# Optimization experiments

Hardware: AMD Instinct MI355X
Metric: run time of the kernel (lower is better)

## Reference

```python
import jax, jax.numpy as jnp
import numpy as np

# module hyper-parameters (init_kwargs)
DELTA_VAR = 0.75
DELTA_DIST = 2.0
ALPHA, BETA, GAMMA = 1.0, 1.0, 0.001

B, E, H, W, C = 4, 16, 512, 512, 24


def _safe_norm(x, axis):
    # L2 norm with zero (not nan) gradient at 0, matching torch.norm's subgradient
    sq = jnp.sum(x * x, axis=axis)
    safe = jnp.where(sq == 0, 1.0, sq)
    return jnp.where(sq == 0, 0.0, jnp.sqrt(safe))


def setup_inputs() -> dict:
    key = jax.random.key(0)
    k1, k2 = jax.random.split(key)
    input_ = jax.random.normal(k1, (B, E, H, W), dtype=jnp.float32)
    target = jax.random.randint(k2, (B, 1, H, W), 0, C)  # consecutive labels 0..C-1 (w.h.p. all present)
    return {"input_": input_, "target": target, "n_instances": C}


def reference(input_, target, n_instances):
    # Discriminative loss (De Brabandere et al. 2017), math identical to the torch
    # one-hot-expansion version but expressed as segment reductions + gathers.
    Cn = int(n_instances)
    b, e = input_.shape[0], input_.shape[1]
    emb = input_.reshape(b, e, -1).transpose(0, 2, 1)  # (B, N, E)
    tgt = target.reshape(b, -1)                        # (B, N) int labels

    # per-instance cluster means: segment-sum over pixels (the torch code does the
    # same reduction via a dense BxCxExHxW one-hot expansion)
    def _means(e_bn, t_n):
        sums = jax.ops.segment_sum(e_bn, t_n, num_segments=Cn)                      # (C, E)
        counts = jax.ops.segment_sum(jnp.ones(t_n.shape, e_bn.dtype), t_n, num_segments=Cn)  # (C,)
        return sums / counts[:, None], counts

    mu, counts = jax.vmap(_means)(emb, tgt)            # (B, C, E), (B, C)

    # variance term: hinged distance of each pixel embedding to its own cluster mean
    mu_per_pix = jnp.take_along_axis(mu, tgt[:, :, None], axis=1)  # (B, N, E)
    dist = _safe_norm(emb - mu_per_pix, axis=-1)                   # (B, N)
    hinge = jnp.square(jnp.maximum(dist - DELTA_VAR, 0.0))
    var_per_inst = jax.vmap(lambda h, t: jax.ops.segment_sum(h, t, num_segments=Cn))(hinge, tgt) / counts  # (B, C)
    variance_term = jnp.mean(jnp.sum(var_per_inst, axis=1) / Cn)

    # distance term: hinged pairwise repulsion between cluster means
    dmat = _safe_norm(mu[:, :, None, :] - mu[:, None, :, :], axis=-1)  # (B, C, C)
    repulsion = 2.0 * DELTA_DIST * (1.0 - jnp.eye(Cn, dtype=mu.dtype))
    hinged = jnp.square(jnp.maximum(repulsion - dmat, 0.0))
    distance_term = jnp.mean(jnp.sum(hinged, axis=(1, 2))) / (Cn * (Cn - 1))

    # regularizer: mean norm of cluster means
    reg_term = jnp.mean(jnp.sum(_safe_norm(mu, axis=-1), axis=1)) / Cn

    return ALPHA * variance_term + BETA * distance_term + GAMMA * reg_term
```

## Files before the change

### kernel.cpp

```cpp
#include <hip/hip_runtime.h>
#include <cstdint>

#define B_SZ   4
#define E_DIM  16
#define C_INST 24
#define HW_N   262144
#define NG     (HW_N / 4)

#define DELTA_VAR  0.75f
#define DELTA_DIST 2.0f
#define ALPHA_W 1.0f
#define BETA_W  1.0f
#define GAMMA_W 0.001f

#define P1_NB   16
#define P1_ITER (NG / (P1_NB * 256))
#define BUK_STRIDE 25

__global__ __launch_bounds__(256) void pass1_kernel(
    const float* __restrict__ input, const int* __restrict__ target,
    float* __restrict__ sums, float* __restrict__ counts)
{
    __shared__ float buk[256][BUK_STRIDE];
    const int tid = threadIdx.x;
    const int eg  = blockIdx.y;
    const int b   = blockIdx.z;

    float* __restrict__ myrow = &buk[tid][0];
    #pragma unroll
    for (int j = 0; j < C_INST; ++j) myrow[j] = 0.f;

    const int4* __restrict__ tgt4 = (const int4*)(target + (size_t)b * HW_N);
    const int gbase = blockIdx.x * 256 * P1_ITER + tid;

    if (eg < E_DIM) {
        const float4* __restrict__ src4 =
            (const float4*)(input + ((size_t)b * E_DIM + eg) * HW_N);
        int4   lab = tgt4[gbase];
        float4 x   = src4[gbase];
        #pragma unroll
        for (int it = 0; it < P1_ITER; ++it) {
            const int4   labc = lab;
            const float4 xc   = x;
            if (it + 1 < P1_ITER) {
                lab = tgt4[gbase + (it + 1) * 256];
                x   = src4[gbase + (it + 1) * 256];
            }
            myrow[labc.x] += xc.x;
            myrow[labc.y] += xc.y;
            myrow[labc.z] += xc.z;
            myrow[labc.w] += xc.w;
        }
    } else {
        #pragma unroll
        for (int it = 0; it < P1_ITER; ++it) {
            const int4 labc = tgt4[gbase + it * 256];
            myrow[labc.x] += 1.f;
            myrow[labc.y] += 1.f;
            myrow[labc.z] += 1.f;
            myrow[labc.w] += 1.f;
        }
    }
    __syncthreads();

    if (tid < 8 * C_INST) {
        const int c  = tid >> 3;
        const int r0 = tid & 7;
        float s = 0.f;
        #pragma unroll
        for (int i = 0; i < 32; ++i) s += buk[8 * i + r0][c];
        s += __shfl_xor(s, 1, 64);
        s += __shfl_xor(s, 2, 64);
        s += __shfl_xor(s, 4, 64);
        if (r0 == 0) {
            if (eg < E_DIM)
                unsafeAtomicAdd(&sums[((size_t)b * E_DIM + eg) * C_INST + c], s);
            else
                unsafeAtomicAdd(&counts[b * C_INST + c], s);
        }
    }
}

__global__ __launch_bounds__(256) void pass2_kernel(
    const float* __restrict__ input, const int* __restrict__ target,
    const float* __restrict__ sums, const float* __restrict__ counts,
    float* __restrict__ loss_acc)
{
    __shared__ float mu_l[C_INST][20];
    __shared__ float w_l[C_INST];
    __shared__ float redw[4];
    const int tid  = threadIdx.x;
    const int lane = tid & 63;
    const int wv   = tid >> 6;
    const int b    = blockIdx.y;

    if (tid < C_INST) {
        const float cv = counts[b * C_INST + tid];
        w_l[tid] = (cv > 0.f) ? 1.f / cv : 0.f;
    }
    __syncthreads();
    for (int i = tid; i < E_DIM * C_INST; i += 256) {
        const int e = i / C_INST, c = i % C_INST;
        mu_l[c][e] = sums[((size_t)b * E_DIM + e) * C_INST + c] * w_l[c];
    }
    __syncthreads();

    const int g = blockIdx.x * 256 + tid;
    const int4 lab4 = ((const int4*)(target + (size_t)b * HW_N))[g];
    const int lp[4] = {lab4.x, lab4.y, lab4.z, lab4.w};

    const float4* __restrict__ src4 = (const float4*)(input + (size_t)b * E_DIM * HW_N);
    float xs[E_DIM * 4];
    #pragma unroll
    for (int e = 0; e < E_DIM; ++e)
        ((float4*)xs)[e] = src4[(size_t)e * NG + g];

    float vloc = 0.f;
    #pragma unroll
    for (int p = 0; p < 4; ++p) {
        const int c = lp[p];
        float d2 = 0.f;
        #pragma unroll
        for (int e = 0; e < E_DIM; ++e) {
            const float diff = xs[e * 4 + p] - mu_l[c][e];
            d2 = fmaf(diff, diff, d2);
        }
        const float h = fmaxf(sqrtf(d2) - DELTA_VAR, 0.f);
        vloc = fmaf(h * h, w_l[c], vloc);
    }

    #pragma unroll
    for (int m = 1; m < 64; m <<= 1) vloc += __shfl_xor(vloc, m, 64);
    if (lane == 0) redw[wv] = vloc;
    __syncthreads();
    if (tid == 0)
        unsafeAtomicAdd(loss_acc, redw[0] + redw[1] + redw[2] + redw[3]);
}

__global__ __launch_bounds__(256) void final_kernel(
    const float* __restrict__ sums, const float* __restrict__ counts,
    const float* __restrict__ loss_acc, float* __restrict__ out)
{
    __shared__ float mu[B_SZ][C_INST][E_DIM];
    __shared__ float red[256];
    const int tid = threadIdx.x;

    for (int i = tid; i < B_SZ * C_INST * E_DIM; i += 256) {
        const int b = i / (C_INST * E_DIM);
        const int r = i % (C_INST * E_DIM);
        const int e = r / C_INST, c = r % C_INST;
        const float cv = counts[b * C_INST + c];
        mu[b][c][e] = (cv > 0.f)
            ? sums[((size_t)b * E_DIM + e) * C_INST + c] / cv : 0.f;
    }
    __syncthreads();

    float acc = 0.f;
    for (int i = tid; i < B_SZ * C_INST; i += 256) {
        const int b = i / C_INST, c = i % C_INST;
        float n2 = 0.f;
        #pragma unroll
        for (int e = 0; e < E_DIM; ++e) n2 += mu[b][c][e] * mu[b][c][e];
        acc += GAMMA_W * sqrtf(n2) * (1.0f / (B_SZ * C_INST));
    }
    for (int i = tid; i < B_SZ * C_INST * C_INST; i += 256) {
        const int b  = i / (C_INST * C_INST);
        const int r  = i % (C_INST * C_INST);
        const int c1 = r / C_INST, c2 = r % C_INST;
        if (c1 != c2) {
            float d2 = 0.f;
            #pragma unroll
            for (int e = 0; e < E_DIM; ++e) {
                const float d = mu[b][c1][e] - mu[b][c2][e];
                d2 += d * d;
            }
            const float h = fmaxf(2.0f * DELTA_DIST - sqrtf(d2), 0.f);
            acc += BETA_W * h * h * (1.0f / (B_SZ * C_INST * (C_INST - 1)));
        }
    }

    red[tid] = acc;
    __syncthreads();
    for (int s = 128; s > 0; s >>= 1) {
        if (tid < s) red[tid] += red[tid + s];
        __syncthreads();
    }
    if (tid == 0)
        out[0] = red[0] + ALPHA_W * loss_acc[0] * (1.0f / (B_SZ * C_INST));
}

extern "C" void kernel_launch(void* const* d_in, const int* in_sizes, int n_in,
                              void* d_out, int out_size, void* d_ws, size_t ws_size,
                              hipStream_t stream)
{
    const float* input  = (const float*)d_in[0];
    const int*   target = (const int*)d_in[1];

    float* sums     = (float*)d_ws;
    float* counts   = sums + B_SZ * E_DIM * C_INST;
    float* loss_acc = counts + B_SZ * C_INST;
    const size_t ws_bytes =
        (size_t)(B_SZ * E_DIM * C_INST + B_SZ * C_INST + 1) * sizeof(float);
    hipMemsetAsync(d_ws, 0, ws_bytes, stream);

    pass1_kernel<<<dim3(P1_NB, E_DIM + 1, B_SZ), 256, 0, stream>>>(input, target, sums, counts);
    pass2_kernel<<<dim3(NG / 256, B_SZ), 256, 0, stream>>>(input, target, sums, counts, loss_acc);
    final_kernel<<<1, 256, 0, stream>>>(sums, counts, loss_acc, (float*)d_out);
}
```

Before: 131.9 us.

## Process two embedding channels per pass1 block and fold counts into ballot popcounts

Each pass1 block now accumulates two embedding channels, so every label load is reused for twice the data and the number of label reads drops. The dedicated count blocks are removed. Instead, each block counts the labels for a slice of iterations using wave ballot and popcount, and the slice is chosen so that the eight channel-pair blocks together cover every chunk exactly once. This costs a larger shared-memory bucket per thread (stride 51), which may lower occupancy, plus ballot overhead in the iterations that do counting.

```diff
diff --git a/kernel.cpp b/kernel.cpp
--- a/kernel.cpp
+++ b/kernel.cpp
@@ -15,69 +15,90 @@
 
 #define P1_NB   16
 #define P1_ITER (NG / (P1_NB * 256))
-#define BUK_STRIDE 25
+#define ROW_STRIDE 51
 
 __global__ __launch_bounds__(256) void pass1_kernel(
     const float* __restrict__ input, const int* __restrict__ target,
     float* __restrict__ sums, float* __restrict__ counts)
 {
-    __shared__ float buk[256][BUK_STRIDE];
-    const int tid = threadIdx.x;
-    const int eg  = blockIdx.y;
-    const int b   = blockIdx.z;
+    __shared__ float buk[256][ROW_STRIDE];
+    __shared__ float crow[4][C_INST];
+    const int tid  = threadIdx.x;
+    const int lane = tid & 63;
+    const int wv   = tid >> 6;
+    const int chunk = blockIdx.x;
+    const int eg2   = blockIdx.y;
+    const int b     = blockIdx.z;
 
     float* __restrict__ myrow = &buk[tid][0];
     #pragma unroll
-    for (int j = 0; j < C_INST; ++j) myrow[j] = 0.f;
+    for (int j = 0; j < 2 * C_INST; ++j) myrow[j] = 0.f;
 
     const int4* __restrict__ tgt4 = (const int4*)(target + (size_t)b * HW_N);
-    const int gbase = blockIdx.x * 256 * P1_ITER + tid;
-
-    if (eg < E_DIM) {
-        const float4* __restrict__ src4 =
-            (const float4*)(input + ((size_t)b * E_DIM + eg) * HW_N);
-        int4   lab = tgt4[gbase];
-        float4 x   = src4[gbase];
-        #pragma unroll
-        for (int it = 0; it < P1_ITER; ++it) {
-            const int4   labc = lab;
-            const float4 xc   = x;
-            if (it + 1 < P1_ITER) {
-                lab = tgt4[gbase + (it + 1) * 256];
-                x   = src4[gbase + (it + 1) * 256];
+    const float4* __restrict__ s0 =
+        (const float4*)(input + ((size_t)b * E_DIM + 2 * eg2) * HW_N);
+    const float4* __restrict__ s1 =
+        (const float4*)(input + ((size_t)b * E_DIM + 2 * eg2 + 1) * HW_N);
+    const int gbase = chunk * 256 * P1_ITER + tid;
+
+    int scnt[C_INST];
+    #pragma unroll
+    for (int c = 0; c < C_INST; ++c) scnt[c] = 0;
+
+    int4   lab = tgt4[gbase];
+    float4 xa  = s0[gbase];
+    float4 xb  = s1[gbase];
+    #pragma unroll
+    for (int it = 0; it < P1_ITER; ++it) {
+        const int4   lc  = lab;
+        const float4 xa0 = xa;
+        const float4 xb0 = xb;
+        if (it + 1 < P1_ITER) {
+            lab = tgt4[gbase + (it + 1) * 256];
+            xa  = s0[gbase + (it + 1) * 256];
+            xb  = s1[gbase + (it + 1) * 256];
+        }
+        myrow[2 * lc.x]     += xa0.x;
+        myrow[2 * lc.x + 1] += xb0.x;
+        myrow[2 * lc.y]     += xa0.y;
+        myrow[2 * lc.y + 1] += xb0.y;
+        myrow[2 * lc.z]     += xa0.z;
+        myrow[2 * lc.z + 1] += xb0.z;
+        myrow[2 * lc.w]     += xa0.w;
+        myrow[2 * lc.w + 1] += xb0.w;
+
+        if ((it >> 1) == eg2) {
+            #pragma unroll
+            for (int c = 0; c < C_INST; ++c) {
+                scnt[c] += (int)__popcll(__ballot(lc.x == c))
+                         + (int)__popcll(__ballot(lc.y == c))
+                         + (int)__popcll(__ballot(lc.z == c))
+                         + (int)__popcll(__ballot(lc.w == c));
             }
-            myrow[labc.x] += xc.x;
-            myrow[labc.y] += xc.y;
-            myrow[labc.z] += xc.z;
-            myrow[labc.w] += xc.w;
-        }
-    } else {
-        #pragma unroll
-        for (int it = 0; it < P1_ITER; ++it) {
-            const int4 labc = tgt4[gbase + it * 256];
-            myrow[labc.x] += 1.f;
-            myrow[labc.y] += 1.f;
-            myrow[labc.z] += 1.f;
-            myrow[labc.w] += 1.f;
-        }
-    }
-    __syncthreads();
-
-    if (tid < 8 * C_INST) {
-        const int c  = tid >> 3;
-        const int r0 = tid & 7;
+        }
+    }
+    if (lane == 0) {
+        #pragma unroll
+        for (int c = 0; c < C_INST; ++c) crow[wv][c] = (float)scnt[c];
+    }
+    __syncthreads();
+
+    if (tid < 4 * 2 * C_INST) {
+        const int j  = tid >> 2;
+        const int r0 = tid & 3;
         float s = 0.f;
         #pragma unroll
-        for (int i = 0; i < 32; ++i) s += buk[8 * i + r0][c];
+        for (int i = 0; i < 64; ++i) s += buk[4 * i + r0][j];
         s += __shfl_xor(s, 1, 64);
         s += __shfl_xor(s, 2, 64);
-        s += __shfl_xor(s, 4, 64);
         if (r0 == 0) {
-            if (eg < E_DIM)
-                unsafeAtomicAdd(&sums[((size_t)b * E_DIM + eg) * C_INST + c], s);
-            else
-                unsafeAtomicAdd(&counts[b * C_INST + c], s);
-        }
+            const int c = j >> 1, d = j & 1;
+            unsafeAtomicAdd(&sums[((size_t)b * E_DIM + 2 * eg2 + d) * C_INST + c], s);
+        }
+    }
+    if (tid < C_INST) {
+        const float s = crow[0][tid] + crow[1][tid] + crow[2][tid] + crow[3][tid];
+        unsafeAtomicAdd(&counts[b * C_INST + tid], s);
     }
 }
 
@@ -122,8 +143,8 @@
         float d2 = 0.f;
         #pragma unroll
         for (int e = 0; e < E_DIM; ++e) {
-            const float diff = xs[e * 4 + p] - mu_l[c][e];
-            d2 = fmaf(diff, diff, d2);
+            const float df = xs[e * 4 + p] - mu_l[c][e];
+            d2 = fmaf(df, df, d2);
         }
         const float h = fmaxf(sqrtf(d2) - DELTA_VAR, 0.f);
         vloc = fmaf(h * h, w_l[c], vloc);
@@ -203,7 +224,7 @@
         (size_t)(B_SZ * E_DIM * C_INST + B_SZ * C_INST + 1) * sizeof(float);
     hipMemsetAsync(d_ws, 0, ws_bytes, stream);
 
-    pass1_kernel<<<dim3(P1_NB, E_DIM + 1, B_SZ), 256, 0, stream>>>(input, target, sums, counts);
+    pass1_kernel<<<dim3(P1_NB, E_DIM / 2, B_SZ), 256, 0, stream>>>(input, target, sums, counts);
     pass2_kernel<<<dim3(NG / 256, B_SZ), 256, 0, stream>>>(input, target, sums, counts, loss_acc);
     final_kernel<<<1, 256, 0, stream>>>(sums, counts, loss_acc, (float*)d_out);
 }
```

Measured after the change: 133.6 us. No clear change (+1.3%).
